# Kernel tuning notes

Hardware: AMD Instinct MI355X
Metric: run time of the kernel (lower is better)

Reference implementation:

```python
import jax, jax.numpy as jnp
import numpy as np

N_NODES = 50000
N_EDGES = 800000
N_GRAPHS = 512
F_IN = 9
H = 64
H2 = 32


def gcn_conv(x, W, b, edge_index, num_nodes):
    # PyG GCNConv: add self loops, sym-normalize, x @ W, scatter-add, + bias
    src, dst = edge_index[0], edge_index[1]
    xw = x @ W  # [N, out]
    deg = 1.0 + jax.ops.segment_sum(jnp.ones_like(src, dtype=xw.dtype), dst,
                                    num_segments=num_nodes)  # self-loop adds 1
    dis = jax.lax.rsqrt(deg)  # deg >= 1
    norm = dis[src] * dis[dst]  # [E]
    out = jax.ops.segment_sum(xw[src] * norm[:, None], dst, num_segments=num_nodes)
    out = out + xw * (dis * dis)[:, None]  # self-loop contribution
    return out + b


def edge_conv(x, W, b, edge_index, num_nodes):
    # PyG EdgeConv with nn = Linear(2*in, out) + ReLU, aggr='max'
    src, dst = edge_index[0], edge_index[1]
    xi = x[dst]
    xj = x[src]
    h = jax.nn.relu(jnp.concatenate([xi, xj - xi], axis=-1) @ W + b)  # [E, out]
    agg = jax.ops.segment_max(h, dst, num_segments=num_nodes)
    return jnp.where(jnp.isfinite(agg), agg, 0.0)  # empty segments -> 0


def setup_inputs() -> dict:
    key = jax.random.key(0)
    ks = jax.random.split(key, 16)
    x = jax.random.normal(ks[0], (N_NODES, F_IN), dtype=jnp.float32)
    edge_index = jax.random.randint(ks[1], (2, N_EDGES), 0, N_NODES, dtype=jnp.int32)
    adj = jax.random.randint(ks[2], (2, N_EDGES), 0, N_NODES, dtype=jnp.int32)
    batch = jnp.sort(jax.random.randint(ks[3], (N_NODES,), 0, N_GRAPHS, dtype=jnp.int32))
    s = lambda fan_in: 1.0 / np.sqrt(fan_in)
    W1 = jax.random.uniform(ks[4], (F_IN, H), jnp.float32, -s(F_IN), s(F_IN))
    b1 = jnp.zeros((H,), jnp.float32)
    eW1 = jax.random.uniform(ks[5], (2 * H, H), jnp.float32, -s(2 * H), s(2 * H))
    eb1 = jnp.zeros((H,), jnp.float32)
    W2 = jax.random.uniform(ks[6], (H, H2), jnp.float32, -s(H), s(H))
    b2 = jnp.zeros((H2,), jnp.float32)
    eW2 = jax.random.uniform(ks[7], (2 * H2, H2), jnp.float32, -s(2 * H2), s(2 * H2))
    eb2 = jnp.zeros((H2,), jnp.float32)
    fcW = jax.random.uniform(ks[8], (H2, 1), jnp.float32, -s(H2), s(H2))
    fcb = jax.random.uniform(ks[9], (1,), jnp.float32, -s(H2), s(H2))
    return {"x": x, "edge_index": edge_index, "adj": adj, "batch": batch,
            "W1": W1, "b1": b1, "eW1": eW1, "eb1": eb1,
            "W2": W2, "b2": b2, "eW2": eW2, "eb2": eb2,
            "fcW": fcW, "fcb": fcb}


def reference(x, edge_index, adj, batch, W1, b1, eW1, eb1, W2, b2, eW2, eb2, fcW, fcb):
    n = x.shape[0]
    h = jax.nn.relu(gcn_conv(x, W1, b1, edge_index, n))
    h = jax.nn.relu(edge_conv(h, eW1, eb1, adj, n))
    h = jax.nn.relu(gcn_conv(h, W2, b2, edge_index, n))
    h = jax.nn.relu(edge_conv(h, eW2, eb2, adj, n))
    h = h @ fcW + fcb  # [N, 1]
    # global_mean_pool
    sums = jax.ops.segment_sum(h, batch, num_segments=N_GRAPHS)
    cnts = jax.ops.segment_sum(jnp.ones((n, 1), h.dtype), batch, num_segments=N_GRAPHS)
    return sums / jnp.maximum(cnts, 1.0)
```

## Files before the change

### kernel.cpp

```cpp
#include <hip/hip_runtime.h>
#include <math.h>

#define NN 50000
#define NE 800000
#define NG 512
#define FIN 9
#define D1 64
#define D2 32
#define PAD 64
#define NN2 (2 * NN)

typedef unsigned long long ull;

static inline int cdiv(int a, int b) { return (a + b - 1) / b; }

__global__ void k_build(const int* __restrict__ ei, const int* __restrict__ adj,
                        int* __restrict__ head_e, ull* __restrict__ pack_e,
                        int* __restrict__ head_a, ull* __restrict__ pack_a) {
  int e = blockIdx.x * blockDim.x + threadIdx.x;
  if (e < NE) {
    int s = ei[e], d = ei[NE + e];
    int nx = atomicExch(&head_e[d], e);
    pack_e[e] = ((ull)(unsigned)s << 32) | (unsigned)nx;
    s = adj[e];
    d = adj[NE + e];
    nx = atomicExch(&head_a[d], e);
    pack_a[e] = ((ull)(unsigned)s << 32) | (unsigned)nx;
  }
}

__global__ void k_convert(const int* __restrict__ head_e, const ull* __restrict__ pack_e,
                          const int* __restrict__ head_a, const ull* __restrict__ pack_a,
                          int* __restrict__ deg_e, int* __restrict__ slot_e,
                          int* __restrict__ deg_a, int* __restrict__ slot_a,
                          float* __restrict__ dis) {
  int t = blockIdx.x * blockDim.x + threadIdx.x;
  if (t >= NN2) return;
  bool isE = t < NN;
  int i = isE ? t : t - NN;
  int e = isE ? head_e[i] : head_a[i];
  const ull* pk = isE ? pack_e : pack_a;
  int* slot = (isE ? slot_e : slot_a) + (size_t)i * PAD;
  int p = 0;
  while (e >= 0 && p < PAD) {
    ull v = pk[e];
    slot[p++] = (int)(v >> 32);
    e = (int)(unsigned)(v & 0xffffffffu);
  }
  (isE ? deg_e : deg_a)[i] = p;
  if (isE) dis[i] = rsqrtf(1.0f + (float)p);
}

__global__ void k_xw1(const float* __restrict__ x, const float* __restrict__ W1,
                      const float* __restrict__ dis, float* __restrict__ xws1) {
  int gid = blockIdx.x * blockDim.x + threadIdx.x;
  int i = gid >> 6, j = gid & 63;
  if (i >= NN) return;
  const float* xr = x + i * FIN;
  float acc = 0.f;
#pragma unroll
  for (int k = 0; k < FIN; ++k) acc += xr[k] * W1[k * D1 + j];
  xws1[i * D1 + j] = acc * dis[i];
}

template <int FI, int FOT, int MODE, bool SCALE>
__global__ __launch_bounds__(256) void k_gemm(const float* __restrict__ H,
                                              const float* __restrict__ W,
                                              const float* __restrict__ dis,
                                              float* __restrict__ OA,
                                              float* __restrict__ OB) {
  constexpr int TM = 4;
  constexpr int TN = (FOT >= 64) ? 4 : 2;
  constexpr int BN = 1024 * TN / FOT;
  constexpr int LDH = BN + 1;
  constexpr int FO = FOT / 2;
  __shared__ float ht[FI][LDH];
  __shared__ float wc[FI][FOT];

  for (int t = threadIdx.x; t < FI * FOT; t += 256) {
    int k = t / FOT, j = t % FOT;
    float v;
    if (MODE == 1)
      v = (j < FO) ? W[k * FO + j] : W[(FI + k) * FO + (j - FO)];
    else
      v = W[k * FOT + j];
    wc[k][j] = v;
  }
  int node0 = blockIdx.x * BN;
  for (int t = threadIdx.x; t < BN * FI; t += 256) {
    int n = t / FI, k = t % FI;
    int nn = node0 + n;
    ht[k][n] = (nn < NN) ? H[(size_t)nn * FI + k] : 0.f;
  }
  __syncthreads();

  int tn = threadIdx.x % (FOT / TN);
  int tm = threadIdx.x / (FOT / TN);
  int j0 = tn * TN, n0 = tm * TM;

  float acc[TM][TN];
#pragma unroll
  for (int m = 0; m < TM; ++m)
#pragma unroll
    for (int q = 0; q < TN; ++q) acc[m][q] = 0.f;

  for (int k = 0; k < FI; ++k) {
    float wv[TN];
    if (TN == 4) {
      float4 w4 = *(const float4*)&wc[k][j0];
      wv[0] = w4.x; wv[1] = w4.y; wv[2] = w4.z; wv[3] = w4.w;
    } else {
      float2 w2 = *(const float2*)&wc[k][j0];
      wv[0] = w2.x; wv[1] = w2.y;
    }
    float hv[TM];
#pragma unroll
    for (int m = 0; m < TM; ++m) hv[m] = ht[k][n0 + m];
#pragma unroll
    for (int m = 0; m < TM; ++m)
#pragma unroll
      for (int q = 0; q < TN; ++q) acc[m][q] += hv[m] * wv[q];
  }

#pragma unroll
  for (int m = 0; m < TM; ++m) {
    int n = node0 + n0 + m;
    if (n >= NN) break;
    float sc = SCALE ? dis[n] : 1.0f;
    float* dst;
    if (MODE == 1)
      dst = (j0 < FO) ? (OA + (size_t)n * FO + j0) : (OB + (size_t)n * FO + (j0 - FO));
    else
      dst = OA + (size_t)n * FOT + j0;
    if (TN == 4) {
      float4 o = {acc[m][0] * sc, acc[m][1] * sc, acc[m][2] * sc, acc[m][3] * sc};
      *(float4*)dst = o;
    } else {
      float2 o = {acc[m][0] * sc, acc[m][1] * sc};
      *(float2*)dst = o;
    }
  }
}

template <int F>
__global__ void k_gcn4(const float4* __restrict__ xws, const float* __restrict__ dis,
                       const int* __restrict__ deg, const int* __restrict__ slots,
                       const float* __restrict__ b, float4* __restrict__ hout) {
  constexpr int L = F / 4;
  int gid = blockIdx.x * blockDim.x + threadIdx.x;
  int i = gid / L, l = gid % L;
  if (i >= NN) return;
  const int* s = slots + (size_t)i * PAD;
  int n = deg[i];
  float4 acc = xws[(size_t)i * L + l];
  int t = 0;
  for (; t + 7 < n; t += 8) {
    int i0 = s[t], i1 = s[t + 1], i2 = s[t + 2], i3 = s[t + 3];
    int i4 = s[t + 4], i5 = s[t + 5], i6 = s[t + 6], i7 = s[t + 7];
    float4 v0 = xws[(size_t)i0 * L + l];
    float4 v1 = xws[(size_t)i1 * L + l];
    float4 v2 = xws[(size_t)i2 * L + l];
    float4 v3 = xws[(size_t)i3 * L + l];
    float4 v4 = xws[(size_t)i4 * L + l];
    float4 v5 = xws[(size_t)i5 * L + l];
    float4 v6 = xws[(size_t)i6 * L + l];
    float4 v7 = xws[(size_t)i7 * L + l];
    acc.x += ((v0.x + v1.x) + (v2.x + v3.x)) + ((v4.x + v5.x) + (v6.x + v7.x));
    acc.y += ((v0.y + v1.y) + (v2.y + v3.y)) + ((v4.y + v5.y) + (v6.y + v7.y));
    acc.z += ((v0.z + v1.z) + (v2.z + v3.z)) + ((v4.z + v5.z) + (v6.z + v7.z));
    acc.w += ((v0.w + v1.w) + (v2.w + v3.w)) + ((v4.w + v5.w) + (v6.w + v7.w));
  }
  for (; t < n; ++t) {
    float4 v = xws[(size_t)s[t] * L + l];
    acc.x += v.x; acc.y += v.y; acc.z += v.z; acc.w += v.w;
  }
  float di = dis[i];
  float4 bb = ((const float4*)b)[l];
  float4 o;
  o.x = fmaxf(bb.x + di * acc.x, 0.f);
  o.y = fmaxf(bb.y + di * acc.y, 0.f);
  o.z = fmaxf(bb.z + di * acc.z, 0.f);
  o.w = fmaxf(bb.w + di * acc.w, 0.f);
  hout[(size_t)i * L + l] = o;
}

template <int F>
__global__ void k_edge4(const float4* __restrict__ A, const float4* __restrict__ B,
                        const float* __restrict__ eb, const int* __restrict__ deg,
                        const int* __restrict__ slots, float4* __restrict__ hout) {
  constexpr int L = F / 4;
  int gid = blockIdx.x * blockDim.x + threadIdx.x;
  int i = gid / L, l = gid % L;
  if (i >= NN) return;
  const int* s = slots + (size_t)i * PAD;
  int n = deg[i];
  float4 M = {-INFINITY, -INFINITY, -INFINITY, -INFINITY};
  int t = 0;
  for (; t + 7 < n; t += 8) {
    int i0 = s[t], i1 = s[t + 1], i2 = s[t + 2], i3 = s[t + 3];
    int i4 = s[t + 4], i5 = s[t + 5], i6 = s[t + 6], i7 = s[t + 7];
    float4 v0 = B[(size_t)i0 * L + l];
    float4 v1 = B[(size_t)i1 * L + l];
    float4 v2 = B[(size_t)i2 * L + l];
    float4 v3 = B[(size_t)i3 * L + l];
    float4 v4 = B[(size_t)i4 * L + l];
    float4 v5 = B[(size_t)i5 * L + l];
    float4 v6 = B[(size_t)i6 * L + l];
    float4 v7 = B[(size_t)i7 * L + l];
    M.x = fmaxf(M.x, fmaxf(fmaxf(fmaxf(v0.x, v1.x), fmaxf(v2.x, v3.x)),
                           fmaxf(fmaxf(v4.x, v5.x), fmaxf(v6.x, v7.x))));
    M.y = fmaxf(M.y, fmaxf(fmaxf(fmaxf(v0.y, v1.y), fmaxf(v2.y, v3.y)),
                           fmaxf(fmaxf(v4.y, v5.y), fmaxf(v6.y, v7.y))));
    M.z = fmaxf(M.z, fmaxf(fmaxf(fmaxf(v0.z, v1.z), fmaxf(v2.z, v3.z)),
                           fmaxf(fmaxf(v4.z, v5.z), fmaxf(v6.z, v7.z))));
    M.w = fmaxf(M.w, fmaxf(fmaxf(fmaxf(v0.w, v1.w), fmaxf(v2.w, v3.w)),
                           fmaxf(fmaxf(v4.w, v5.w), fmaxf(v6.w, v7.w))));
  }
  for (; t < n; ++t) {
    float4 v = B[(size_t)s[t] * L + l];
    M.x = fmaxf(M.x, v.x); M.y = fmaxf(M.y, v.y);
    M.z = fmaxf(M.z, v.z); M.w = fmaxf(M.w, v.w);
  }
  float4 a = A[(size_t)i * L + l];
  float4 bsl = B[(size_t)i * L + l];
  float4 e4 = ((const float4*)eb)[l];
  float4 o;
  o.x = fmaxf(a.x - bsl.x + e4.x + M.x, 0.f);
  o.y = fmaxf(a.y - bsl.y + e4.y + M.y, 0.f);
  o.z = fmaxf(a.z - bsl.z + e4.z + M.z, 0.f);
  o.w = fmaxf(a.w - bsl.w + e4.w + M.w, 0.f);
  hout[(size_t)i * L + l] = o;
}

__global__ void k_final(const float* __restrict__ h4, const float* __restrict__ fcW,
                        const float* __restrict__ fcb, const int* __restrict__ batch,
                        float* __restrict__ sums, float* __restrict__ cnt) {
  int i = blockIdx.x * blockDim.x + threadIdx.x;
  int lane = threadIdx.x & 63;
  bool valid = (i < NN);
  float val = 0.f, c = 0.f;
  int g = -1;
  if (valid) {
    float acc = fcb[0];
#pragma unroll
    for (int k = 0; k < D2; ++k) acc += h4[(size_t)i * D2 + k] * fcW[k];
    val = acc;
    c = 1.f;
    g = batch[i];
  }
#pragma unroll
  for (int d = 1; d < 64; d <<= 1) {
    float v2 = __shfl_down(val, d);
    float c2 = __shfl_down(c, d);
    int g2 = __shfl_down(g, d);
    if (lane + d < 64 && g2 == g) {
      val += v2;
      c += c2;
    }
  }
  int gprev = __shfl_up(g, 1);
  bool is_head = (lane == 0) || (gprev != g);
  if (valid && is_head) {
    atomicAdd(&sums[g], val);
    atomicAdd(&cnt[g], c);
  }
}

__global__ void k_out(const float* __restrict__ sums, const float* __restrict__ cnt,
                      float* __restrict__ out) {
  int g = blockIdx.x * blockDim.x + threadIdx.x;
  if (g < NG) out[g] = sums[g] / fmaxf(cnt[g], 1.0f);
}

extern "C" void kernel_launch(void* const* d_in, const int* in_sizes, int n_in,
                              void* d_out, int out_size, void* d_ws, size_t ws_size,
                              hipStream_t stream) {
  const float* x = (const float*)d_in[0];
  const int* ei = (const int*)d_in[1];
  const int* adj = (const int*)d_in[2];
  const int* batch = (const int*)d_in[3];
  const float* W1 = (const float*)d_in[4];
  const float* b1 = (const float*)d_in[5];
  const float* eW1 = (const float*)d_in[6];
  const float* eb1 = (const float*)d_in[7];
  const float* W2 = (const float*)d_in[8];
  const float* b2 = (const float*)d_in[9];
  const float* eW2 = (const float*)d_in[10];
  const float* eb2 = (const float*)d_in[11];
  const float* fcW = (const float*)d_in[12];
  const float* fcb = (const float*)d_in[13];
  float* out = (float*)d_out;

  char* ws = (char*)d_ws;
  size_t p = 0;
  auto alloc = [&](size_t bytes) -> void* {
    void* r = ws + p;
    p = (p + bytes + 255) & ~(size_t)255;
    return r;
  };
  int* head_e = (int*)alloc(NN * 4);
  int* head_a = (int*)alloc(NN * 4);
  size_t ff_bytes = p;
  float* sums = (float*)alloc(NG * 4);
  float* cnt = (float*)alloc(NG * 4);
  size_t zero_end = p;
  ull* pack_e = (ull*)alloc((size_t)NE * 8);
  ull* pack_a = (ull*)alloc((size_t)NE * 8);
  int* deg_e = (int*)alloc(NN * 4);
  int* deg_a = (int*)alloc(NN * 4);
  int* slot_e = (int*)alloc((size_t)NN * PAD * 4);
  int* slot_a = (int*)alloc((size_t)NN * PAD * 4);
  float* dis = (float*)alloc(NN * 4);
  float* buf0 = (float*)alloc((size_t)NN * D1 * 4);
  float* buf1 = (float*)alloc((size_t)NN * D1 * 4);
  float* buf2 = (float*)alloc((size_t)NN * D1 * 4);
  float* buf3 = (float*)alloc((size_t)NN * D1 * 4);

  hipMemsetAsync(d_ws, 0xFF, ff_bytes, stream);
  hipMemsetAsync(ws + ff_bytes, 0, zero_end - ff_bytes, stream);

  k_build<<<cdiv(NE, 256), 256, 0, stream>>>(ei, adj, head_e, pack_e, head_a, pack_a);
  k_convert<<<cdiv(NN2, 256), 256, 0, stream>>>(head_e, pack_e, head_a, pack_a,
                                                deg_e, slot_e, deg_a, slot_a, dis);

  k_xw1<<<cdiv(NN * D1, 256), 256, 0, stream>>>(x, W1, dis, buf0);
  k_gcn4<D1><<<cdiv(NN * (D1 / 4), 256), 256, 0, stream>>>(
      (const float4*)buf0, dis, deg_e, slot_e, b1, (float4*)buf1);

  k_gemm<D1, 2 * D1, 1, false><<<cdiv(NN, 32), 256, 0, stream>>>(buf1, eW1, nullptr, buf2, buf3);
  k_edge4<D1><<<cdiv(NN * (D1 / 4), 256), 256, 0, stream>>>(
      (const float4*)buf2, (const float4*)buf3, eb1, deg_a, slot_a, (float4*)buf0);

  k_gemm<D1, D2, 0, true><<<cdiv(NN, 64), 256, 0, stream>>>(buf0, W2, dis, buf1, nullptr);
  k_gcn4<D2><<<cdiv(NN * (D2 / 4), 256), 256, 0, stream>>>(
      (const float4*)buf1, dis, deg_e, slot_e, b2, (float4*)buf3);

  float* A2 = buf2;
  float* B2 = buf2 + (size_t)NN * D2;
  k_gemm<D2, 2 * D2, 1, false><<<cdiv(NN, 64), 256, 0, stream>>>(buf3, eW2, nullptr, A2, B2);
  k_edge4<D2><<<cdiv(NN * (D2 / 4), 256), 256, 0, stream>>>(
      (const float4*)A2, (const float4*)B2, eb2, deg_a, slot_a, (float4*)buf1);

  k_final<<<cdiv(NN, 256), 256, 0, stream>>>(buf1, fcW, fcb, batch, sums, cnt);
  k_out<<<cdiv(NG, 256), 256, 0, stream>>>(sums, cnt, out);
}
```

Before: 374.6 us.

## Aggregate raw 9-dim features before first GCN matmul

Reorders the first GCN layer so the neighbour aggregation runs on the dis-scaled 9-wide input (padded to 16) instead of on the 64-wide product x@W1. The matmul with W1, the dis scaling, bias and ReLU then run afterwards in a new gemm mode. This cuts the gather traffic of the first aggregation by about a factor of four. The cost is an extra padded feature buffer and a different floating-point summation order.

```diff
diff --git a/kernel.cpp b/kernel.cpp
--- a/kernel.cpp
+++ b/kernel.cpp
@@ -9,6 +9,7 @@
 #define D2 32
 #define PAD 64
 #define NN2 (2 * NN)
+#define XSP 16
 
 typedef unsigned long long ull;
 
@@ -31,9 +32,10 @@
 
 __global__ void k_convert(const int* __restrict__ head_e, const ull* __restrict__ pack_e,
                           const int* __restrict__ head_a, const ull* __restrict__ pack_a,
+                          const float* __restrict__ x,
                           int* __restrict__ deg_e, int* __restrict__ slot_e,
                           int* __restrict__ deg_a, int* __restrict__ slot_a,
-                          float* __restrict__ dis) {
+                          float* __restrict__ dis, float* __restrict__ xs) {
   int t = blockIdx.x * blockDim.x + threadIdx.x;
   if (t >= NN2) return;
   bool isE = t < NN;
@@ -48,25 +50,56 @@
     e = (int)(unsigned)(v & 0xffffffffu);
   }
   (isE ? deg_e : deg_a)[i] = p;
-  if (isE) dis[i] = rsqrtf(1.0f + (float)p);
-}
-
-__global__ void k_xw1(const float* __restrict__ x, const float* __restrict__ W1,
-                      const float* __restrict__ dis, float* __restrict__ xws1) {
+  if (isE) {
+    float di = rsqrtf(1.0f + (float)p);
+    dis[i] = di;
+    const float* xr = x + (size_t)i * FIN;
+    float* xo = xs + (size_t)i * XSP;
+#pragma unroll
+    for (int k = 0; k < FIN; ++k) xo[k] = xr[k] * di;
+#pragma unroll
+    for (int k = FIN; k < XSP; ++k) xo[k] = 0.f;
+  }
+}
+
+__global__ void k_gagg(const float4* __restrict__ xs, const int* __restrict__ deg,
+                       const int* __restrict__ slots, float4* __restrict__ g) {
+  constexpr int L = XSP / 4;
   int gid = blockIdx.x * blockDim.x + threadIdx.x;
-  int i = gid >> 6, j = gid & 63;
+  int i = gid / L, l = gid % L;
   if (i >= NN) return;
-  const float* xr = x + i * FIN;
-  float acc = 0.f;
-#pragma unroll
-  for (int k = 0; k < FIN; ++k) acc += xr[k] * W1[k * D1 + j];
-  xws1[i * D1 + j] = acc * dis[i];
-}
-
-template <int FI, int FOT, int MODE, bool SCALE>
+  const int* s = slots + (size_t)i * PAD;
+  int n = deg[i];
+  float4 acc = xs[(size_t)i * L + l];
+  int t = 0;
+  for (; t + 7 < n; t += 8) {
+    int i0 = s[t], i1 = s[t + 1], i2 = s[t + 2], i3 = s[t + 3];
+    int i4 = s[t + 4], i5 = s[t + 5], i6 = s[t + 6], i7 = s[t + 7];
+    float4 v0 = xs[(size_t)i0 * L + l];
+    float4 v1 = xs[(size_t)i1 * L + l];
+    float4 v2 = xs[(size_t)i2 * L + l];
+    float4 v3 = xs[(size_t)i3 * L + l];
+    float4 v4 = xs[(size_t)i4 * L + l];
+    float4 v5 = xs[(size_t)i5 * L + l];
+    float4 v6 = xs[(size_t)i6 * L + l];
+    float4 v7 = xs[(size_t)i7 * L + l];
+    acc.x += ((v0.x + v1.x) + (v2.x + v3.x)) + ((v4.x + v5.x) + (v6.x + v7.x));
+    acc.y += ((v0.y + v1.y) + (v2.y + v3.y)) + ((v4.y + v5.y) + (v6.y + v7.y));
+    acc.z += ((v0.z + v1.z) + (v2.z + v3.z)) + ((v4.z + v5.z) + (v6.z + v7.z));
+    acc.w += ((v0.w + v1.w) + (v2.w + v3.w)) + ((v4.w + v5.w) + (v6.w + v7.w));
+  }
+  for (; t < n; ++t) {
+    float4 v = xs[(size_t)s[t] * L + l];
+    acc.x += v.x; acc.y += v.y; acc.z += v.z; acc.w += v.w;
+  }
+  g[(size_t)i * L + l] = acc;
+}
+
+template <int FI, int FOT, int MODE, bool SCALE, int LDHS>
 __global__ __launch_bounds__(256) void k_gemm(const float* __restrict__ H,
                                               const float* __restrict__ W,
                                               const float* __restrict__ dis,
+                                              const float* __restrict__ bias,
                                               float* __restrict__ OA,
                                               float* __restrict__ OB) {
   constexpr int TM = 4;
@@ -90,7 +123,7 @@
   for (int t = threadIdx.x; t < BN * FI; t += 256) {
     int n = t / FI, k = t % FI;
     int nn = node0 + n;
-    ht[k][n] = (nn < NN) ? H[(size_t)nn * FI + k] : 0.f;
+    ht[k][n] = (nn < NN) ? H[(size_t)nn * LDHS + k] : 0.f;
   }
   __syncthreads();
 
@@ -126,18 +159,27 @@
   for (int m = 0; m < TM; ++m) {
     int n = node0 + n0 + m;
     if (n >= NN) break;
-    float sc = SCALE ? dis[n] : 1.0f;
+    float o[TN];
+    if (MODE == 2) {
+      float di = dis[n];
+#pragma unroll
+      for (int q = 0; q < TN; ++q) o[q] = fmaxf(bias[j0 + q] + di * acc[m][q], 0.f);
+    } else {
+      float sc = SCALE ? dis[n] : 1.0f;
+#pragma unroll
+      for (int q = 0; q < TN; ++q) o[q] = acc[m][q] * sc;
+    }
     float* dst;
     if (MODE == 1)
       dst = (j0 < FO) ? (OA + (size_t)n * FO + j0) : (OB + (size_t)n * FO + (j0 - FO));
     else
       dst = OA + (size_t)n * FOT + j0;
     if (TN == 4) {
-      float4 o = {acc[m][0] * sc, acc[m][1] * sc, acc[m][2] * sc, acc[m][3] * sc};
-      *(float4*)dst = o;
+      float4 ov = {o[0], o[1], o[2], o[3]};
+      *(float4*)dst = ov;
     } else {
-      float2 o = {acc[m][0] * sc, acc[m][1] * sc};
-      *(float2*)dst = o;
+      float2 ov = {o[0], o[1]};
+      *(float2*)dst = ov;
     }
   }
 }
@@ -311,6 +353,8 @@
   int* slot_e = (int*)alloc((size_t)NN * PAD * 4);
   int* slot_a = (int*)alloc((size_t)NN * PAD * 4);
   float* dis = (float*)alloc(NN * 4);
+  float* xs = (float*)alloc((size_t)NN * XSP * 4);
+  float* gbuf = (float*)alloc((size_t)NN * XSP * 4);
   float* buf0 = (float*)alloc((size_t)NN * D1 * 4);
   float* buf1 = (float*)alloc((size_t)NN * D1 * 4);
   float* buf2 = (float*)alloc((size_t)NN * D1 * 4);
@@ -320,24 +364,28 @@
   hipMemsetAsync(ws + ff_bytes, 0, zero_end - ff_bytes, stream);
 
   k_build<<<cdiv(NE, 256), 256, 0, stream>>>(ei, adj, head_e, pack_e, head_a, pack_a);
-  k_convert<<<cdiv(NN2, 256), 256, 0, stream>>>(head_e, pack_e, head_a, pack_a,
-                                                deg_e, slot_e, deg_a, slot_a, dis);
-
-  k_xw1<<<cdiv(NN * D1, 256), 256, 0, stream>>>(x, W1, dis, buf0);
-  k_gcn4<D1><<<cdiv(NN * (D1 / 4), 256), 256, 0, stream>>>(
-      (const float4*)buf0, dis, deg_e, slot_e, b1, (float4*)buf1);
-
-  k_gemm<D1, 2 * D1, 1, false><<<cdiv(NN, 32), 256, 0, stream>>>(buf1, eW1, nullptr, buf2, buf3);
+  k_convert<<<cdiv(NN2, 256), 256, 0, stream>>>(head_e, pack_e, head_a, pack_a, x,
+                                                deg_e, slot_e, deg_a, slot_a, dis, xs);
+
+  k_gagg<<<cdiv(NN * (XSP / 4), 256), 256, 0, stream>>>(
+      (const float4*)xs, deg_e, slot_e, (float4*)gbuf);
+  k_gemm<FIN, D1, 2, false, XSP><<<cdiv(NN, 64), 256, 0, stream>>>(
+      gbuf, W1, dis, b1, buf1, nullptr);
+
+  k_gemm<D1, 2 * D1, 1, false, D1><<<cdiv(NN, 32), 256, 0, stream>>>(
+      buf1, eW1, nullptr, nullptr, buf2, buf3);
   k_edge4<D1><<<cdiv(NN * (D1 / 4), 256), 256, 0, stream>>>(
       (const float4*)buf2, (const float4*)buf3, eb1, deg_a, slot_a, (float4*)buf0);
 
-  k_gemm<D1, D2, 0, true><<<cdiv(NN, 64), 256, 0, stream>>>(buf0, W2, dis, buf1, nullptr);
+  k_gemm<D1, D2, 0, true, D1><<<cdiv(NN, 64), 256, 0, stream>>>(
+      buf0, W2, dis, nullptr, buf1, nullptr);
   k_gcn4<D2><<<cdiv(NN * (D2 / 4), 256), 256, 0, stream>>>(
       (const float4*)buf1, dis, deg_e, slot_e, b2, (float4*)buf3);
 
   float* A2 = buf2;
   float* B2 = buf2 + (size_t)NN * D2;
-  k_gemm<D2, 2 * D2, 1, false><<<cdiv(NN, 64), 256, 0, stream>>>(buf3, eW2, nullptr, A2, B2);
+  k_gemm<D2, 2 * D2, 1, false, D2><<<cdiv(NN, 64), 256, 0, stream>>>(
+      buf3, eW2, nullptr, nullptr, A2, B2);
   k_edge4<D2><<<cdiv(NN * (D2 / 4), 256), 256, 0, stream>>>(
       (const float4*)A2, (const float4*)B2, eb2, deg_a, slot_a, (float4*)buf1);
 
```

Result: faster. 352.1 us (-6.0%).
